# Performance work log

Measured on AMD Instinct MI355X. Metric: run time of the kernel, lower is better.

Reference implementation:

```python
import jax, jax.numpy as jnp
import numpy as np

B, S, D, H = 2, 2048, 1024, 16
HD = D // H  # head_dim = 64


def setup_inputs() -> dict:
    key = jax.random.key(0)
    ks = jax.random.split(key, 9)
    sc = 1.0 / np.sqrt(D)
    return {
        "X": jax.random.normal(ks[0], (B, S, D), jnp.float32),
        "Wq": jax.random.normal(ks[1], (D, D), jnp.float32) * sc,
        "bq": jnp.zeros((D,), jnp.float32),
        "Wk": jax.random.normal(ks[2], (D, D), jnp.float32) * sc,
        "bk": jnp.zeros((D,), jnp.float32),
        "Wv": jax.random.normal(ks[3], (D, D), jnp.float32) * sc,
        "bv": jnp.zeros((D,), jnp.float32),
        "Wo": jax.random.normal(ks[4], (D, D), jnp.float32) * sc,
        "bo": jnp.zeros((D,), jnp.float32),
    }


def reference(X, Wq, bq, Wk, bk, Wv, bv, Wo, bo):
    b, s, d = X.shape
    q = (X @ Wq + bq).reshape(b, s, H, HD).transpose(0, 2, 1, 3)  # [B,H,S,HD]
    k = (X @ Wk + bk).reshape(b, s, H, HD).transpose(0, 2, 1, 3)
    v = (X @ Wv + bv).reshape(b, s, H, HD).transpose(0, 2, 1, 3)
    score = jnp.einsum("bhqd,bhkd->bhqk", q, k) / jnp.sqrt(jnp.float32(HD))
    causal = jnp.tril(jnp.ones((s, s), bool))  # [S,S]
    score = jnp.where(causal[None, None], score, -jnp.inf)
    attn = jax.nn.softmax(score, axis=-1)
    out = jnp.einsum("bhqk,bhkd->bhqd", attn, v)  # [B,H,S,HD]
    out = out.transpose(0, 2, 1, 3).reshape(b, s, d)
    return out @ Wo + bo
```

## Files before the change

### kernel.cpp

```cpp
#include <hip/hip_runtime.h>
#include <hip/hip_bf16.h>
#include <math.h>

#define B_SZ 2
#define S_SZ 2048
#define D_SZ 1024
#define H_SZ 16
#define HD_SZ 64
constexpr int M_ROWS = B_SZ * S_SZ;

typedef __bf16 bf16x8 __attribute__((ext_vector_type(8)));
typedef __bf16 bf16x4 __attribute__((ext_vector_type(4)));
typedef float f32x4 __attribute__((ext_vector_type(4)));

#define GLOAD_LDS16(gsrc, ldst)                                              \
  __builtin_amdgcn_global_load_lds(                                          \
      (const __attribute__((address_space(1))) void*)(gsrc),                 \
      (__attribute__((address_space(3))) void*)(ldst), 16, 0, 0)

__global__ __launch_bounds__(256) void prep_all(const float* __restrict__ X,
                                                const float* __restrict__ W0,
                                                const float* __restrict__ W1,
                                                const float* __restrict__ W2,
                                                const float* __restrict__ W3,
                                                __bf16* __restrict__ Xb,
                                                __bf16* __restrict__ Wt) {
  __shared__ float Ts[32][33];
  const int z = blockIdx.z;
  if (z < 4) {
    const float* W = z == 0 ? W0 : (z == 1 ? W1 : (z == 2 ? W2 : W3));
    __bf16* out = Wt + (size_t)z * 1024 * 1024;
    const int k0 = blockIdx.x * 32, n0 = blockIdx.y * 32;
    const int tr = threadIdx.x >> 3;
    const int tc = (threadIdx.x & 7) * 4;
    const float4 v =
        *reinterpret_cast<const float4*>(&W[(size_t)(k0 + tr) * 1024 + n0 + tc]);
    Ts[tr][tc + 0] = v.x;
    Ts[tr][tc + 1] = v.y;
    Ts[tr][tc + 2] = v.z;
    Ts[tr][tc + 3] = v.w;
    __syncthreads();
    bf16x4 o;
#pragma unroll
    for (int j = 0; j < 4; ++j) o[j] = (__bf16)Ts[tc + j][tr];
    *reinterpret_cast<bf16x4*>(&out[(size_t)(n0 + tr) * 1024 + k0 + tc]) = o;
  } else {
    const int flat = blockIdx.y * 32 + blockIdx.x;
    const size_t e0 = ((size_t)flat * 256 + threadIdx.x) * 16;
#pragma unroll
    for (int half = 0; half < 2; ++half) {
      const float4 a = *reinterpret_cast<const float4*>(&X[e0 + half * 8]);
      const float4 b = *reinterpret_cast<const float4*>(&X[e0 + half * 8 + 4]);
      bf16x8 o;
      o[0] = (__bf16)a.x; o[1] = (__bf16)a.y; o[2] = (__bf16)a.z; o[3] = (__bf16)a.w;
      o[4] = (__bf16)b.x; o[5] = (__bf16)b.y; o[6] = (__bf16)b.z; o[7] = (__bf16)b.w;
      *reinterpret_cast<bf16x8*>(&Xb[e0 + half * 8]) = o;
    }
  }
}

__global__ __launch_bounds__(256) void transpose_v(const __bf16* __restrict__ V,
                                                   __bf16* __restrict__ Vt) {
  constexpr int TST = 66;
  __shared__ __bf16 T[64 * TST];
  const int bh = blockIdx.y;
  const int s0 = blockIdx.x * 64;
  const size_t base = (size_t)bh * S_SZ * HD_SZ;
  const int tid = threadIdx.x;
  for (int i = tid; i < 512; i += 256) {
    const int r = i >> 3, c = (i & 7) * 8;
    *reinterpret_cast<bf16x8*>(&T[r * TST + c]) =
        *reinterpret_cast<const bf16x8*>(&V[base + (size_t)(s0 + r) * 64 + c]);
  }
  __syncthreads();
  const size_t obase = (size_t)bh * HD_SZ * S_SZ;
  for (int i = tid; i < 512; i += 256) {
    const int d = i >> 3, c = (i & 7) * 8;
    bf16x8 o;
#pragma unroll
    for (int j = 0; j < 8; ++j) o[j] = T[(c + j) * TST + d];
    *reinterpret_cast<bf16x8*>(&Vt[obase + (size_t)d * S_SZ + s0 + c]) = o;
  }
}

template <int MODE, int BN>
__global__ __launch_bounds__(256) void gemm_mfma(
    const __bf16* __restrict__ Ab, const __bf16* __restrict__ Bt,
    const float* __restrict__ bias0, const float* __restrict__ bias1,
    const float* __restrict__ bias2, float* __restrict__ C0,
    __bf16* __restrict__ Q0, __bf16* __restrict__ K0, __bf16* __restrict__ V0,
    int M, int N, int K) {
  constexpr int NJ = BN / 32;
  __shared__ __bf16 As[2][128 * 32];
  __shared__ __bf16 Bs[2][BN * 32];
  __shared__ __bf16 Ep[(MODE == 1) ? 32 * 132 : 4];

  const int tid = threadIdx.x;
  const int lane = tid & 63;
  const int w = tid >> 6;
  const int lr = lane & 15, lg = lane >> 4;
  const int wr = w >> 1, wc = w & 1;
  const int bm = blockIdx.x * 128;
  const int bn = blockIdx.y * BN;

  const int r0 = tid >> 2, c0 = (tid & 3) * 8;
  const int r1 = (tid + 256) >> 2, c1 = ((tid + 256) & 3) * 8;
  const __bf16* aS0 = &Ab[(size_t)(bm + r0) * K + c0];
  const __bf16* aS1 = &Ab[(size_t)(bm + r1) * K + c1];
  const __bf16* bS0 = &Bt[(size_t)(bn + r0) * K + c0];
  const __bf16* bS1 = &Bt[(size_t)(bn + r1) * K + c1];

  f32x4 acc[4][NJ] = {};

  auto STAGE = [&](int buf) {
    GLOAD_LDS16(aS0, &As[buf][w * 512]);
    GLOAD_LDS16(aS1, &As[buf][2048 + w * 512]);
    GLOAD_LDS16(bS0, &Bs[buf][w * 512]);
    if constexpr (BN == 128) GLOAD_LDS16(bS1, &Bs[buf][2048 + w * 512]);
    aS0 += 32; aS1 += 32; bS0 += 32;
    if constexpr (BN == 128) bS1 += 32;
  };

  STAGE(0);
  asm volatile("s_waitcnt vmcnt(0)" ::: "memory");
  __builtin_amdgcn_s_barrier();
  __builtin_amdgcn_sched_barrier(0);
  int cur = 0;

  for (int k0 = 0; k0 < K; k0 += 32) {
    const bool has_next = (k0 + 32 < K);
    if (has_next) STAGE(cur ^ 1);
    if (k0) {
      if (has_next) {
        if constexpr (BN == 128)
          asm volatile("s_waitcnt vmcnt(4)" ::: "memory");
        else
          asm volatile("s_waitcnt vmcnt(3)" ::: "memory");
      } else {
        asm volatile("s_waitcnt vmcnt(0)" ::: "memory");
      }
      __builtin_amdgcn_s_barrier();
      __builtin_amdgcn_sched_barrier(0);
    }

    bf16x8 af[4], bfr[NJ];
#pragma unroll
    for (int i = 0; i < 4; ++i)
      af[i] = *reinterpret_cast<const bf16x8*>(&As[cur][(wr * 64 + i * 16 + lr) * 32 + lg * 8]);
#pragma unroll
    for (int j = 0; j < NJ; ++j)
      bfr[j] = *reinterpret_cast<const bf16x8*>(&Bs[cur][(wc * (BN / 2) + j * 16 + lr) * 32 + lg * 8]);
    __builtin_amdgcn_s_setprio(1);
#pragma unroll
    for (int i = 0; i < 4; ++i)
#pragma unroll
      for (int j = 0; j < NJ; ++j)
        acc[i][j] = __builtin_amdgcn_mfma_f32_16x16x32_bf16(af[i], bfr[j], acc[i][j], 0, 0, 0);
    __builtin_amdgcn_s_setprio(0);
    __builtin_amdgcn_sched_barrier(0);
    __builtin_amdgcn_s_barrier();
    cur ^= 1;
  }

  if (MODE == 0) {
#pragma unroll
    for (int j = 0; j < NJ; ++j) {
      const int n = bn + wc * (BN / 2) + j * 16 + lr;
      const float bs = bias0[n];
#pragma unroll
      for (int i = 0; i < 4; ++i) {
        const int mrow = bm + wr * 64 + i * 16 + lg * 4;
#pragma unroll
        for (int r = 0; r < 4; ++r)
          C0[(size_t)(mrow + r) * N + n] = acc[i][j][r] + bs;
      }
    }
  } else {
    const int which = bn >> 10;
    __bf16* dst = which == 0 ? Q0 : (which == 1 ? K0 : V0);
    const float* bp = which == 0 ? bias0 : (which == 1 ? bias1 : bias2);
    const float scale = which == 0 ? 0.18033688011112042f : 1.0f;
    float bias4[4];
#pragma unroll
    for (int j = 0; j < 4; ++j)
      bias4[j] = bp[(bn & 1023) + wc * 64 + j * 16 + lr];

#pragma unroll
    for (int i = 0; i < 4; ++i) {
      __syncthreads();
#pragma unroll
      for (int j = 0; j < 4; ++j) {
        const int colw = wc * 64 + j * 16 + lr;
#pragma unroll
        for (int r = 0; r < 4; ++r)
          Ep[(wr * 16 + lg * 4 + r) * 132 + colw] =
              (__bf16)((acc[i][j][r] + bias4[j]) * scale);
      }
      __syncthreads();
#pragma unroll
      for (int u = 0; u < 2; ++u) {
        const int c = tid + u * 256;
        const int er = c >> 4;
        const int off = (c & 15) * 8;
        const int m = bm + (er >> 4) * 64 + i * 16 + (er & 15);
        const int nn = (bn & 1023) + off;
        const int hh = nn >> 6, hd = nn & 63;
        const int bb = m >> 11, ss = m & (S_SZ - 1);
        *reinterpret_cast<bf16x8*>(
            &dst[(((size_t)(bb * H_SZ + hh)) * S_SZ + ss) * HD_SZ + hd]) =
            *reinterpret_cast<const bf16x8*>(&Ep[er * 132 + off]);
      }
    }
  }
}

__global__ __launch_bounds__(256) void attn_mfma(const __bf16* __restrict__ Q,
                                                 const __bf16* __restrict__ Kg,
                                                 const __bf16* __restrict__ Vtg,
                                                 __bf16* __restrict__ Aout) {
  constexpr int PST = 76;
  __shared__ __bf16 Ks[2][64 * 64];
  __shared__ __bf16 Vts[64 * 64];
  __shared__ __bf16 Ps[4][16 * PST];

  const int tid = threadIdx.x;
  const int lane = tid & 63;
  const int w = tid >> 6;
  const int lr = lane & 15;
  const int lg = lane >> 4;

  const int flat = blockIdx.x;
  const int g = flat >> 5;
  const int r8 = g & 7, j4 = g >> 3;
  const int qb = (j4 == 0) ? r8 : (j4 == 1) ? (15 - r8)
                                : (j4 == 2) ? (16 + r8) : (31 - r8);
  const int hb = flat & 31;
  const int h = hb >> 1, b = hb & 1;
  const size_t base = (size_t)(b * H_SZ + h) * S_SZ * HD_SZ;
  const int q0 = qb * 64 + w * 16;

  bf16x8 aq[2];
#pragma unroll
  for (int hh = 0; hh < 2; ++hh)
    aq[hh] = *reinterpret_cast<const bf16x8*>(
        &Q[base + (size_t)(q0 + lr) * 64 + hh * 32 + lg * 8]);

  const int srow = lane >> 3;
  const int schunk = (lane & 7) ^ srow;

  bf16x8 ones8;
#pragma unroll
  for (int j = 0; j < 8; ++j) ones8[j] = (__bf16)1.0f;

  f32x4 oacc[4] = {};
  f32x4 oacc_l = {};

  const int ntiles = qb + 1;

  const int rbA = w * 16, rbB = w * 16 + 8;
  const __bf16* kS0 = &Kg[base + (size_t)(rbA + srow) * 64 + schunk * 8];
  const __bf16* kS1 = &Kg[base + (size_t)(rbB + srow) * 64 + schunk * 8];
  const __bf16* vS0 = &Vtg[base + (size_t)(rbA + srow) * S_SZ + schunk * 8];
  const __bf16* vS1 = &Vtg[base + (size_t)(rbB + srow) * S_SZ + schunk * 8];

  GLOAD_LDS16(kS0, &Ks[0][rbA * 64]);
  GLOAD_LDS16(kS1, &Ks[0][rbB * 64]);
  int cur = 0;

  for (int t0 = 0; t0 < ntiles; ++t0) {
    asm volatile("s_waitcnt vmcnt(0)" ::: "memory");
    __builtin_amdgcn_s_barrier();
    __builtin_amdgcn_sched_barrier(0);

    GLOAD_LDS16(vS0, &Vts[rbA * 64]);
    GLOAD_LDS16(vS1, &Vts[rbB * 64]);
    vS0 += 64; vS1 += 64;
    const bool has_next = (t0 + 1 < ntiles);
    if (has_next) {
      kS0 += 64 * 64; kS1 += 64 * 64;
      GLOAD_LDS16(kS0, &Ks[cur ^ 1][rbA * 64]);
      GLOAD_LDS16(kS1, &Ks[cur ^ 1][rbB * 64]);
    }

    f32x4 s[4];
    __builtin_amdgcn_s_setprio(1);
#pragma unroll
    for (int t = 0; t < 4; ++t) {
      const int row = t * 16 + lr;
      const bf16x8 k0f = *reinterpret_cast<const bf16x8*>(
          &Ks[cur][row * 64 + ((lg ^ (lr & 7)) * 8)]);
      const bf16x8 k1f = *reinterpret_cast<const bf16x8*>(
          &Ks[cur][row * 64 + (((4 | lg) ^ (lr & 7)) * 8)]);
      f32x4 z = (f32x4){0.f, 0.f, 0.f, 0.f};
      z = __builtin_amdgcn_mfma_f32_16x16x32_bf16(aq[0], k0f, z, 0, 0, 0);
      z = __builtin_amdgcn_mfma_f32_16x16x32_bf16(aq[1], k1f, z, 0, 0, 0);
      s[t] = z;
    }
    __builtin_amdgcn_s_setprio(0);

    if (t0 == qb) {
#pragma unroll
      for (int t = 0; t < 4; ++t) {
        const int key = t0 * 64 + t * 16 + lr;
#pragma unroll
        for (int r = 0; r < 4; ++r) {
          const int qrow = q0 + lg * 4 + r;
          if (key > qrow) s[t][r] = -INFINITY;
        }
      }
    }

#pragma unroll
    for (int t = 0; t < 4; ++t)
#pragma unroll
      for (int r = 0; r < 4; ++r)
        Ps[w][(lg * 4 + r) * PST + t * 16 + lr] =
            (__bf16)__builtin_amdgcn_exp2f(s[t][r]);
    asm volatile("s_waitcnt lgkmcnt(0)" ::: "memory");
    __builtin_amdgcn_sched_barrier(0);

    if (has_next)
      asm volatile("s_waitcnt vmcnt(2)" ::: "memory");
    else
      asm volatile("s_waitcnt vmcnt(0)" ::: "memory");
    __builtin_amdgcn_s_barrier();
    __builtin_amdgcn_sched_barrier(0);

    __builtin_amdgcn_s_setprio(1);
#pragma unroll
    for (int kh = 0; kh < 2; ++kh) {
      const bf16x8 pa = *reinterpret_cast<const bf16x8*>(
          &Ps[w][lr * PST + kh * 32 + lg * 8]);
#pragma unroll
      for (int dc = 0; dc < 4; ++dc) {
        const int row = dc * 16 + lr;
        const bf16x8 vf = *reinterpret_cast<const bf16x8*>(
            &Vts[row * 64 + (((kh * 4 + lg) ^ (lr & 7)) * 8)]);
        oacc[dc] = __builtin_amdgcn_mfma_f32_16x16x32_bf16(pa, vf, oacc[dc], 0, 0, 0);
      }
      oacc_l = __builtin_amdgcn_mfma_f32_16x16x32_bf16(pa, ones8, oacc_l, 0, 0, 0);
    }
    __builtin_amdgcn_s_setprio(0);
    __builtin_amdgcn_sched_barrier(0);
    cur ^= 1;
  }

#pragma unroll
  for (int r = 0; r < 4; ++r) {
    const float inv = 1.f / oacc_l[r];
#pragma unroll
    for (int dc = 0; dc < 4; ++dc)
      Ps[w][(lg * 4 + r) * PST + dc * 16 + lr] = (__bf16)(oacc[dc][r] * inv);
  }
  asm volatile("s_waitcnt lgkmcnt(0)" ::: "memory");
  __builtin_amdgcn_sched_barrier(0);
#pragma unroll
  for (int u = 0; u < 2; ++u) {
    const int c = lane + u * 64;
    const int row = c >> 3;
    const int off = (c & 7) * 8;
    const int qg = q0 + row;
    *reinterpret_cast<bf16x8*>(
        &Aout[(size_t)(b * S_SZ + qg) * D_SZ + h * 64 + off]) =
        *reinterpret_cast<const bf16x8*>(&Ps[w][row * PST + off]);
  }
}

extern "C" void kernel_launch(void* const* d_in, const int* in_sizes, int n_in,
                              void* d_out, int out_size, void* d_ws,
                              size_t ws_size, hipStream_t stream) {
  const float* X = (const float*)d_in[0];
  const float* Wq = (const float*)d_in[1];
  const float* bq = (const float*)d_in[2];
  const float* Wk = (const float*)d_in[3];
  const float* bk = (const float*)d_in[4];
  const float* Wv = (const float*)d_in[5];
  const float* bv = (const float*)d_in[6];
  const float* Wo = (const float*)d_in[7];
  const float* bo = (const float*)d_in[8];
  float* out = (float*)d_out;

  const size_t elems = (size_t)M_ROWS * D_SZ;
  const size_t welems = (size_t)D_SZ * D_SZ;
  __bf16* Xb = (__bf16*)d_ws;
  __bf16* Wt = Xb + elems;
  __bf16* Q = Wt + 4 * welems;
  __bf16* K = Q + elems;
  __bf16* V = K + elems;
  __bf16* Vt = V + elems;
  __bf16* Ahb = Vt + elems;

  prep_all<<<dim3(32, 32, 5), 256, 0, stream>>>(X, Wq, Wk, Wv, Wo, Xb, Wt);

  gemm_mfma<1, 128><<<dim3(M_ROWS / 128, 3072 / 128), 256, 0, stream>>>(
      Xb, Wt, bq, bk, bv, nullptr, Q, K, V, M_ROWS, 3072, D_SZ);

  transpose_v<<<dim3(32, 32), 256, 0, stream>>>(V, Vt);

  attn_mfma<<<dim3(1024), 256, 0, stream>>>(Q, K, Vt, Ahb);

  gemm_mfma<0, 64><<<dim3(M_ROWS / 128, D_SZ / 64), 256, 0, stream>>>(
      Ahb, Wt + 3 * welems, bo, nullptr, nullptr, out, nullptr, nullptr,
      nullptr, M_ROWS, D_SZ, D_SZ);
}
```

Measured before the change: 112.8 us.

## Fuse V transpose into QKV epilogue and double-buffer V in attention

```diff
diff --git a/kernel.cpp b/kernel.cpp
--- a/kernel.cpp
+++ b/kernel.cpp
@@ -59,30 +59,6 @@
   }
 }
 
-__global__ __launch_bounds__(256) void transpose_v(const __bf16* __restrict__ V,
-                                                   __bf16* __restrict__ Vt) {
-  constexpr int TST = 66;
-  __shared__ __bf16 T[64 * TST];
-  const int bh = blockIdx.y;
-  const int s0 = blockIdx.x * 64;
-  const size_t base = (size_t)bh * S_SZ * HD_SZ;
-  const int tid = threadIdx.x;
-  for (int i = tid; i < 512; i += 256) {
-    const int r = i >> 3, c = (i & 7) * 8;
-    *reinterpret_cast<bf16x8*>(&T[r * TST + c]) =
-        *reinterpret_cast<const bf16x8*>(&V[base + (size_t)(s0 + r) * 64 + c]);
-  }
-  __syncthreads();
-  const size_t obase = (size_t)bh * HD_SZ * S_SZ;
-  for (int i = tid; i < 512; i += 256) {
-    const int d = i >> 3, c = (i & 7) * 8;
-    bf16x8 o;
-#pragma unroll
-    for (int j = 0; j < 8; ++j) o[j] = T[(c + j) * TST + d];
-    *reinterpret_cast<bf16x8*>(&Vt[obase + (size_t)d * S_SZ + s0 + c]) = o;
-  }
-}
-
 template <int MODE, int BN>
 __global__ __launch_bounds__(256) void gemm_mfma(
     const __bf16* __restrict__ Ab, const __bf16* __restrict__ Bt,
@@ -93,7 +69,7 @@
   constexpr int NJ = BN / 32;
   __shared__ __bf16 As[2][128 * 32];
   __shared__ __bf16 Bs[2][BN * 32];
-  __shared__ __bf16 Ep[(MODE == 1) ? 32 * 132 : 4];
+  __shared__ __bf16 Ep[(MODE == 1) ? 128 * 40 : 4];
 
   const int tid = threadIdx.x;
   const int lane = tid & 63;
@@ -177,7 +153,6 @@
     }
   } else {
     const int which = bn >> 10;
-    __bf16* dst = which == 0 ? Q0 : (which == 1 ? K0 : V0);
     const float* bp = which == 0 ? bias0 : (which == 1 ? bias1 : bias2);
     const float scale = which == 0 ? 0.18033688011112042f : 1.0f;
     float bias4[4];
@@ -185,30 +160,58 @@
     for (int j = 0; j < 4; ++j)
       bias4[j] = bp[(bn & 1023) + wc * 64 + j * 16 + lr];
 
-#pragma unroll
-    for (int i = 0; i < 4; ++i) {
-      __syncthreads();
-#pragma unroll
-      for (int j = 0; j < 4; ++j) {
-        const int colw = wc * 64 + j * 16 + lr;
-#pragma unroll
-        for (int r = 0; r < 4; ++r)
-          Ep[(wr * 16 + lg * 4 + r) * 132 + colw] =
-              (__bf16)((acc[i][j][r] + bias4[j]) * scale);
-      }
-      __syncthreads();
-#pragma unroll
-      for (int u = 0; u < 2; ++u) {
-        const int c = tid + u * 256;
-        const int er = c >> 4;
-        const int off = (c & 15) * 8;
-        const int m = bm + (er >> 4) * 64 + i * 16 + (er & 15);
-        const int nn = (bn & 1023) + off;
+    if (which < 2) {
+      __bf16* dst = which == 0 ? Q0 : K0;
+#pragma unroll
+      for (int i = 0; i < 4; ++i) {
+        __syncthreads();
+#pragma unroll
+        for (int j = 0; j < 4; ++j) {
+          const int colw = wc * 64 + j * 16 + lr;
+#pragma unroll
+          for (int r = 0; r < 4; ++r)
+            Ep[(wr * 16 + lg * 4 + r) * 132 + colw] =
+                (__bf16)((acc[i][j][r] + bias4[j]) * scale);
+        }
+        __syncthreads();
+#pragma unroll
+        for (int u = 0; u < 2; ++u) {
+          const int c = tid + u * 256;
+          const int er = c >> 4;
+          const int off = (c & 15) * 8;
+          const int m = bm + (er >> 4) * 64 + i * 16 + (er & 15);
+          const int nn = (bn & 1023) + off;
+          const int hh = nn >> 6, hd = nn & 63;
+          const int bb = m >> 11, ss = m & (S_SZ - 1);
+          *reinterpret_cast<bf16x8*>(
+              &dst[(((size_t)(bb * H_SZ + hh)) * S_SZ + ss) * HD_SZ + hd]) =
+              *reinterpret_cast<const bf16x8*>(&Ep[er * 132 + off]);
+        }
+      }
+    } else {
+#pragma unroll
+      for (int i = 0; i < 4; ++i) {
+        __syncthreads();
+#pragma unroll
+        for (int j = 0; j < 4; ++j) {
+          const int colw = wc * 64 + j * 16 + lr;
+#pragma unroll
+          for (int r = 0; r < 4; ++r)
+            Ep[colw * 40 + wr * 16 + lg * 4 + r] =
+                (__bf16)(acc[i][j][r] + bias4[j]);
+        }
+        __syncthreads();
+        const int col = tid & 127, r2 = tid >> 7;
+        const int nn = (bn & 1023) + col;
         const int hh = nn >> 6, hd = nn & 63;
-        const int bb = m >> 11, ss = m & (S_SZ - 1);
-        *reinterpret_cast<bf16x8*>(
-            &dst[(((size_t)(bb * H_SZ + hh)) * S_SZ + ss) * HD_SZ + hd]) =
-            *reinterpret_cast<const bf16x8*>(&Ep[er * 132 + off]);
+        const int m0 = bm + r2 * 64 + i * 16;
+        const int bb = m0 >> 11, ss0 = m0 & (S_SZ - 1);
+        __bf16* dstp =
+            &V0[(((size_t)(bb * H_SZ + hh)) * HD_SZ + hd) * S_SZ + ss0];
+        *reinterpret_cast<bf16x8*>(dstp) =
+            *reinterpret_cast<const bf16x8*>(&Ep[col * 40 + r2 * 16]);
+        *reinterpret_cast<bf16x8*>(dstp + 8) =
+            *reinterpret_cast<const bf16x8*>(&Ep[col * 40 + r2 * 16 + 8]);
       }
     }
   }
@@ -220,7 +223,7 @@
                                                  __bf16* __restrict__ Aout) {
   constexpr int PST = 76;
   __shared__ __bf16 Ks[2][64 * 64];
-  __shared__ __bf16 Vts[64 * 64];
+  __shared__ __bf16 Vts[2][64 * 64];
   __shared__ __bf16 Ps[4][16 * PST];
 
   const int tid = threadIdx.x;
@@ -231,9 +234,7 @@
 
   const int flat = blockIdx.x;
   const int g = flat >> 5;
-  const int r8 = g & 7, j4 = g >> 3;
-  const int qb = (j4 == 0) ? r8 : (j4 == 1) ? (15 - r8)
-                                : (j4 == 2) ? (16 + r8) : (31 - r8);
+  const int qb = (g < 16) ? (31 - g) : (g - 16);
   const int hb = flat & 31;
   const int h = hb >> 1, b = hb & 1;
   const size_t base = (size_t)(b * H_SZ + h) * S_SZ * HD_SZ;
@@ -263,8 +264,14 @@
   const __bf16* vS0 = &Vtg[base + (size_t)(rbA + srow) * S_SZ + schunk * 8];
   const __bf16* vS1 = &Vtg[base + (size_t)(rbB + srow) * S_SZ + schunk * 8];
 
-  GLOAD_LDS16(kS0, &Ks[0][rbA * 64]);
-  GLOAD_LDS16(kS1, &Ks[0][rbB * 64]);
+  auto ISSUE = [&](int buf) {
+    GLOAD_LDS16(kS0, &Ks[buf][rbA * 64]);
+    GLOAD_LDS16(kS1, &Ks[buf][rbB * 64]);
+    GLOAD_LDS16(vS0, &Vts[buf][rbA * 64]);
+    GLOAD_LDS16(vS1, &Vts[buf][rbB * 64]);
+  };
+
+  ISSUE(0);
   int cur = 0;
 
   for (int t0 = 0; t0 < ntiles; ++t0) {
@@ -272,14 +279,10 @@
     __builtin_amdgcn_s_barrier();
     __builtin_amdgcn_sched_barrier(0);
 
-    GLOAD_LDS16(vS0, &Vts[rbA * 64]);
-    GLOAD_LDS16(vS1, &Vts[rbB * 64]);
-    vS0 += 64; vS1 += 64;
-    const bool has_next = (t0 + 1 < ntiles);
-    if (has_next) {
+    if (t0 + 1 < ntiles) {
       kS0 += 64 * 64; kS1 += 64 * 64;
-      GLOAD_LDS16(kS0, &Ks[cur ^ 1][rbA * 64]);
-      GLOAD_LDS16(kS1, &Ks[cur ^ 1][rbB * 64]);
+      vS0 += 64;      vS1 += 64;
+      ISSUE(cur ^ 1);
     }
 
     f32x4 s[4];
@@ -319,13 +322,6 @@
     asm volatile("s_waitcnt lgkmcnt(0)" ::: "memory");
     __builtin_amdgcn_sched_barrier(0);
 
-    if (has_next)
-      asm volatile("s_waitcnt vmcnt(2)" ::: "memory");
-    else
-      asm volatile("s_waitcnt vmcnt(0)" ::: "memory");
-    __builtin_amdgcn_s_barrier();
-    __builtin_amdgcn_sched_barrier(0);
-
     __builtin_amdgcn_s_setprio(1);
 #pragma unroll
     for (int kh = 0; kh < 2; ++kh) {
@@ -335,7 +331,7 @@
       for (int dc = 0; dc < 4; ++dc) {
         const int row = dc * 16 + lr;
         const bf16x8 vf = *reinterpret_cast<const bf16x8*>(
-            &Vts[row * 64 + (((kh * 4 + lg) ^ (lr & 7)) * 8)]);
+            &Vts[cur][row * 64 + (((kh * 4 + lg) ^ (lr & 7)) * 8)]);
         oacc[dc] = __builtin_amdgcn_mfma_f32_16x16x32_bf16(pa, vf, oacc[dc], 0, 0, 0);
       }
       oacc_l = __builtin_amdgcn_mfma_f32_16x16x32_bf16(pa, ones8, oacc_l, 0, 0, 0);
@@ -386,16 +382,13 @@
   __bf16* Wt = Xb + elems;
   __bf16* Q = Wt + 4 * welems;
   __bf16* K = Q + elems;
-  __bf16* V = K + elems;
-  __bf16* Vt = V + elems;
+  __bf16* Vt = K + elems;
   __bf16* Ahb = Vt + elems;
 
   prep_all<<<dim3(32, 32, 5), 256, 0, stream>>>(X, Wq, Wk, Wv, Wo, Xb, Wt);
 
   gemm_mfma<1, 128><<<dim3(M_ROWS / 128, 3072 / 128), 256, 0, stream>>>(
-      Xb, Wt, bq, bk, bv, nullptr, Q, K, V, M_ROWS, 3072, D_SZ);
-
-  transpose_v<<<dim3(32, 32), 256, 0, stream>>>(V, Vt);
+      Xb, Wt, bq, bk, bv, nullptr, Q, K, Vt, M_ROWS, 3072, D_SZ);
 
   attn_mfma<<<dim3(1024), 256, 0, stream>>>(Q, K, Vt, Ahb);
 
```

Result: faster. 106.4 us (-5.6%).
